# Kernel optimization log

Hardware: AMD Instinct MI355X
Metric: run time of the kernel (lower is better)

The kernel has to match this reference:

```python
import jax, jax.numpy as jnp
import numpy as np

D_MODEL = 512
NUM_HEADS = 8
D_HEAD = 64
BATCH = 2
SEQ = 2048
NEG_BIG = 1.0e10


def setup_inputs() -> dict:
    key = jax.random.key(0)
    k1, k2, k3, k4, k5 = jax.random.split(key, 5)
    scale = D_MODEL ** -0.5
    return {
        "x": jax.random.normal(k1, (BATCH, SEQ, D_MODEL), dtype=jnp.float32),
        "W_Q": jax.random.normal(k2, (NUM_HEADS, D_HEAD, D_MODEL), dtype=jnp.float32) * scale,
        "W_K": jax.random.normal(k3, (NUM_HEADS, D_HEAD, D_MODEL), dtype=jnp.float32) * scale,
        "W_V": jax.random.normal(k4, (NUM_HEADS, D_HEAD, D_MODEL), dtype=jnp.float32) * scale,
        "W_O": jax.random.normal(k5, (D_MODEL, D_HEAD * NUM_HEADS), dtype=jnp.float32) * scale,
    }


def reference(x, W_Q, W_K, W_V, W_O):
    b, n, d = x.shape
    # q,k,v: [b, heads, pos, d_head]
    q = jnp.einsum('ihd,bpd->biph', W_Q, x)
    k = jnp.einsum('ihd,bpd->biph', W_K, x)
    v = jnp.einsum('ihd,bpd->biph', W_V, x)
    # scores: [b, heads, q_pos, k_pos]
    scores = jnp.einsum('biph,biqh->biqp', k, q)
    tril = jnp.tril(jnp.ones((n, n), dtype=scores.dtype))   # keep p <= q
    triu = jnp.triu(jnp.ones((n, n), dtype=scores.dtype))   # buffer 'mask'
    # Faithful to source: tril(scores) - 1e10 * (1 - triu)
    masked = scores * tril - NEG_BIG * (1.0 - triu)
    attn = jax.nn.softmax(masked / (D_HEAD ** 0.5), axis=-1)
    z = jnp.einsum('biph,biqp->biqh', v, attn)               # [b, i, q, h]
    z_flat = jnp.transpose(z, (0, 2, 1, 3)).reshape(b, n, -1)  # [b, q, i*h]
    out = jnp.einsum('df,bqf->bqd', W_O, z_flat)
    return out
```

## Files before the change

### kernel.cpp

```cpp
#include <hip/hip_runtime.h>
#include <stdint.h>

#define BATCH 2
#define SEQ 2048
#define DM 512
#define NH 8
#define DH 64
#define MROWS (BATCH * SEQ)
#define NCHUNK 64
#define CHUNK (SEQ / NCHUNK)

typedef __attribute__((ext_vector_type(8))) short bf16x8;
typedef __attribute__((ext_vector_type(4))) float f32x4;

__device__ __forceinline__ unsigned short f2bf(float f) {
    union { float f; uint32_t u; } x; x.f = f;
    uint32_t r = x.u + 0x7fffu + ((x.u >> 16) & 1u);
    return (unsigned short)(r >> 16);
}
__device__ __forceinline__ float bf2f(unsigned short s) {
    union { uint32_t u; float f; } x; x.u = ((uint32_t)s) << 16;
    return x.f;
}

__device__ __forceinline__ void gl_lds16(const void* g, void* l) {
    __builtin_amdgcn_global_load_lds(
        (const __attribute__((address_space(1))) void*)(uintptr_t)g,
        (__attribute__((address_space(3))) void*)(uint32_t)(uintptr_t)l,
        16, 0, 0);
}

__global__ void cvt_all(const float4* __restrict__ x,
                        const float4* __restrict__ Wq, const float4* __restrict__ Wk,
                        const float4* __restrict__ Wv, const float4* __restrict__ Wo,
                        ushort4* __restrict__ xb, ushort4* __restrict__ wb) {
    int i = blockIdx.x * blockDim.x + threadIdx.x;
    float4 v; ushort4* dst; int off;
    if (i < 524288) {
        v = x[i]; dst = xb; off = i;
    } else {
        int j = i - 524288;
        if (j < 131072) {
            int head = j >> 14, rp = (j >> 7) & 127, colq = j & 127;
            v = (rp < 64) ? Wq[head * 8192 + rp * 128 + colq]
                          : Wk[head * 8192 + (rp - 64) * 128 + colq];
        } else if (j < 196608) {
            v = Wv[j - 131072];
        } else {
            v = Wo[j - 196608];
        }
        dst = wb; off = j;
    }
    ushort4 o; o.x = f2bf(v.x); o.y = f2bf(v.y); o.z = f2bf(v.z); o.w = f2bf(v.w);
    dst[off] = o;
}

__global__ __launch_bounds__(256) void proj(
    const unsigned short* __restrict__ xb, const unsigned short* __restrict__ wb,
    float* __restrict__ cA, float* __restrict__ cW,
    unsigned short* __restrict__ V, float* __restrict__ csum)
{
    __shared__ __align__(16) unsigned short S[4 * 256 * 32];
    const int t = threadIdx.x, lane = t & 63, wave = t >> 6;
    const int lr2 = lane >> 2;
    const int csrc = ((lane & 3) ^ ((lane >> 3) & 3)) * 8;
    const int l15 = lane & 15, q = lane >> 4;
    const int bid = blockIdx.x;
    const int wm = wave * 32;

    if (bid < 256) {
        constexpr int TE = 256 * 32;
        const int head = bid & 7, m0 = (bid >> 3) * 128;
        const unsigned short* Bw = wb + head * 65536;
        const unsigned short* gb[4];
#pragma unroll
        for (int r = 0; r < 4; r++) {
            int g = (r * 4 + wave) * 16 + lr2;
            gb[r] = (g < 128) ? xb + (size_t)(m0 + g) * 512 + csrc
                              : Bw + (size_t)(g - 128) * 512 + csrc;
        }
        int aoff[2], boff[8];
#pragma unroll
        for (int i = 0; i < 2; i++) {
            int R = wm + i * 16 + l15;
            aoff[i] = R * 32 + ((q ^ ((R >> 1) & 3)) * 8);
        }
#pragma unroll
        for (int j = 0; j < 8; j++) {
            int R = 128 + j * 16 + l15;
            boff[j] = R * 32 + ((q ^ ((R >> 1) & 3)) * 8);
        }
        f32x4 acc[2][8];
#pragma unroll
        for (int i = 0; i < 2; i++)
#pragma unroll
            for (int j = 0; j < 8; j++) { f32x4 z = {0.f,0.f,0.f,0.f}; acc[i][j] = z; }

        auto stage = [&](int buf, int tt) {
            const int k0 = tt * 32;
#pragma unroll
            for (int r = 0; r < 4; r++)
                gl_lds16(gb[r] + k0, S + buf * TE + (r * 4 + wave) * 512);
        };
        auto compute = [&](int buf) {
            const unsigned short* Sb = S + buf * TE;
            bf16x8 af[2], bfr[8];
#pragma unroll
            for (int i = 0; i < 2; i++) af[i] = *(const bf16x8*)(Sb + aoff[i]);
#pragma unroll
            for (int j = 0; j < 8; j++) bfr[j] = *(const bf16x8*)(Sb + boff[j]);
            __builtin_amdgcn_s_setprio(1);
#pragma unroll
            for (int i = 0; i < 2; i++)
#pragma unroll
                for (int j = 0; j < 8; j++)
                    acc[i][j] = __builtin_amdgcn_mfma_f32_16x16x32_bf16(af[i], bfr[j], acc[i][j], 0, 0, 0);
            __builtin_amdgcn_s_setprio(0);
        };

        stage(0, 0); stage(1, 1); stage(2, 2);
        for (int tt = 0; tt < 14; ++tt) {
            asm volatile("s_waitcnt vmcnt(8)" ::: "memory");
            __builtin_amdgcn_s_barrier();
            compute(tt & 3);
            if (tt <= 12) stage((tt + 3) & 3, tt + 3);
        }
        asm volatile("s_waitcnt vmcnt(4)" ::: "memory");
        __builtin_amdgcn_s_barrier();
        compute(2);
        asm volatile("s_waitcnt vmcnt(0)" ::: "memory");
        __builtin_amdgcn_s_barrier();
        compute(3);

#pragma unroll
        for (int i = 0; i < 2; i++)
#pragma unroll
            for (int r = 0; r < 4; r++) {
                float d = 0.f;
#pragma unroll
                for (int j = 0; j < 4; j++) d += acc[i][j][r] * acc[i][j + 4][r];
                d += __shfl_xor(d, 1); d += __shfl_xor(d, 2);
                d += __shfl_xor(d, 4); d += __shfl_xor(d, 8);
                if (l15 == 0) {
                    int row = m0 + wm + i * 16 + (lane >> 4) * 4 + r;
                    int p = row & (SEQ - 1);
                    float dd = d * 0.125f;
                    float M = fmaxf(dd, 0.f);
                    float a = expf(dd - M), e0 = expf(-M);
                    float Z = a + (float)(SEQ - 1 - p) * e0;
                    cA[row * NH + head] = a / Z;
                    cW[row * NH + head] = e0 / Z;
                }
            }
    } else {
        constexpr int TE2 = 192 * 32;
        const int b2 = bid - 256;
        const int head = b2 & 7, m0 = (b2 >> 3) * 128, n0 = head * 64;
        const unsigned short* Bv = wb + 524288 + (size_t)n0 * 512;
        const unsigned short* gb[3];
#pragma unroll
        for (int r = 0; r < 3; r++) {
            int g = (r * 4 + wave) * 16 + lr2;
            gb[r] = (g < 128) ? xb + (size_t)(m0 + g) * 512 + csrc
                              : Bv + (size_t)(g - 128) * 512 + csrc;
        }
        int aoff[2], boff[4];
#pragma unroll
        for (int i = 0; i < 2; i++) {
            int R = wm + i * 16 + l15;
            aoff[i] = R * 32 + ((q ^ ((R >> 1) & 3)) * 8);
        }
#pragma unroll
        for (int j = 0; j < 4; j++) {
            int R = 128 + j * 16 + l15;
            boff[j] = R * 32 + ((q ^ ((R >> 1) & 3)) * 8);
        }
        f32x4 acc[2][4];
#pragma unroll
        for (int i = 0; i < 2; i++)
#pragma unroll
            for (int j = 0; j < 4; j++) { f32x4 z = {0.f,0.f,0.f,0.f}; acc[i][j] = z; }

        auto stage = [&](int buf, int tt) {
            const int k0 = tt * 32;
#pragma unroll
            for (int r = 0; r < 3; r++)
                gl_lds16(gb[r] + k0, S + buf * TE2 + (r * 4 + wave) * 512);
        };
        auto compute = [&](int buf) {
            const unsigned short* Sb = S + buf * TE2;
            bf16x8 af[2], bfr[4];
#pragma unroll
            for (int i = 0; i < 2; i++) af[i] = *(const bf16x8*)(Sb + aoff[i]);
#pragma unroll
            for (int j = 0; j < 4; j++) bfr[j] = *(const bf16x8*)(Sb + boff[j]);
            __builtin_amdgcn_s_setprio(1);
#pragma unroll
            for (int i = 0; i < 2; i++)
#pragma unroll
                for (int j = 0; j < 4; j++)
                    acc[i][j] = __builtin_amdgcn_mfma_f32_16x16x32_bf16(af[i], bfr[j], acc[i][j], 0, 0, 0);
            __builtin_amdgcn_s_setprio(0);
        };

        stage(0, 0); stage(1, 1); stage(2, 2);
        for (int tt = 0; tt < 14; ++tt) {
            asm volatile("s_waitcnt vmcnt(6)" ::: "memory");
            __builtin_amdgcn_s_barrier();
            compute(tt & 3);
            if (tt <= 12) stage((tt + 3) & 3, tt + 3);
        }
        asm volatile("s_waitcnt vmcnt(3)" ::: "memory");
        __builtin_amdgcn_s_barrier();
        compute(2);
        asm volatile("s_waitcnt vmcnt(0)" ::: "memory");
        __builtin_amdgcn_s_barrier();
        compute(3);

        const int crow = m0 + wm + (lane >> 4) * 4;
#pragma unroll
        for (int i = 0; i < 2; i++)
#pragma unroll
            for (int j = 0; j < 4; j++)
#pragma unroll
                for (int r = 0; r < 4; r++)
                    V[(size_t)(crow + i * 16 + r) * DM + n0 + j * 16 + l15] = f2bf(acc[i][j][r]);
        float s[4];
#pragma unroll
        for (int j = 0; j < 4; j++) {
            s[j] = 0.f;
#pragma unroll
            for (int i = 0; i < 2; i++)
#pragma unroll
                for (int r = 0; r < 4; r++) s[j] += acc[i][j][r];
            s[j] += __shfl_xor(s[j], 16);
            s[j] += __shfl_xor(s[j], 32);
        }
        if (lane < 16) {
            int bi = (m0 >> 11) * NH + head;
            int chunk = ((m0 & (SEQ - 1)) >> 5) + wave;
#pragma unroll
            for (int j = 0; j < 4; j++)
                csum[(bi * NCHUNK + chunk) * 64 + j * 16 + lane] = s[j];
        }
    }
}

__global__ __launch_bounds__(256) void zbuild(
    const unsigned short* __restrict__ V, const float* __restrict__ csum,
    const float* __restrict__ cA, const float* __restrict__ cW,
    unsigned short* __restrict__ Zb) {
    int ci = blockIdx.x * 4 + (threadIdx.x >> 6);
    int h = threadIdx.x & 63;
    int c = ci & (NCHUNK - 1), bi = ci >> 6;
    int i = bi & 7, b = bi >> 3;
    float r = 0.f;
#pragma unroll 4
    for (int cc = c + 1; cc < NCHUNK; cc++) r += csum[((bi << 6) + cc) * 64 + h];
#pragma unroll 4
    for (int j = CHUNK - 1; j >= 0; j--) {
        int p = c * CHUNK + j;
        size_t row = (size_t)(b * SEQ + p);
        float v = bf2f(V[row * DM + i * DH + h]);
        float a = cA[row * NH + i], w = cW[row * NH + i];
        Zb[row * DM + i * DH + h] = f2bf(fmaf(a, v, w * r));
        r += v;
    }
}

template<int TM, int TN, int WM, int WN>
__global__ __launch_bounds__(256) void gemm_bt(
    const unsigned short* __restrict__ A, const unsigned short* __restrict__ B,
    float* __restrict__ C, int M, int N, int K)
{
    constexpr int ROWS = TM + TN;
    static_assert(ROWS == 128, "pipeline waits assume 128 staged rows");
    constexpr int MI = WM / 16, NJ = WN / 16;
    constexpr int WAVES_N = TN / WN;
    constexpr int TE = ROWS * 32;
    __shared__ __align__(16) unsigned short S[4 * TE];
    const int t = threadIdx.x, lane = t & 63, wave = t >> 6;
    const int wm = (wave / WAVES_N) * WM, wn = (wave % WAVES_N) * WN;
    const int m0 = blockIdx.x * TM, n0 = blockIdx.y * TN;
    const int lr2 = lane >> 2;
    const int csrc = ((lane & 3) ^ ((lane >> 3) & 3)) * 8;
    const int l15 = lane & 15, q = lane >> 4;

    const unsigned short* gb[2];
#pragma unroll
    for (int r = 0; r < 2; r++) {
        int g = (r * 4 + wave) * 16 + lr2;
        gb[r] = (g < TM) ? A + (size_t)(m0 + g) * K + csrc
                         : B + (size_t)(n0 + g - TM) * K + csrc;
    }
    int aoff[MI], boff[NJ];
#pragma unroll
    for (int i = 0; i < MI; i++) {
        int R = wm + i * 16 + l15;
        aoff[i] = R * 32 + ((q ^ ((R >> 1) & 3)) * 8);
    }
#pragma unroll
    for (int j = 0; j < NJ; j++) {
        int R = TM + wn + j * 16 + l15;
        boff[j] = R * 32 + ((q ^ ((R >> 1) & 3)) * 8);
    }

    f32x4 acc[MI][NJ];
#pragma unroll
    for (int i = 0; i < MI; i++)
#pragma unroll
        for (int j = 0; j < NJ; j++) { f32x4 z = {0.f,0.f,0.f,0.f}; acc[i][j] = z; }

    auto stage = [&](int buf, int tt) {
        const int k0 = tt * 32;
#pragma unroll
        for (int r = 0; r < 2; r++)
            gl_lds16(gb[r] + k0, S + buf * TE + (r * 4 + wave) * 512);
    };
    auto compute = [&](int buf) {
        const unsigned short* Sb = S + buf * TE;
        bf16x8 af[MI], bfr[NJ];
#pragma unroll
        for (int i = 0; i < MI; i++) af[i] = *(const bf16x8*)(Sb + aoff[i]);
#pragma unroll
        for (int j = 0; j < NJ; j++) bfr[j] = *(const bf16x8*)(Sb + boff[j]);
        __builtin_amdgcn_s_setprio(1);
#pragma unroll
        for (int i = 0; i < MI; i++)
#pragma unroll
            for (int j = 0; j < NJ; j++)
                acc[i][j] = __builtin_amdgcn_mfma_f32_16x16x32_bf16(af[i], bfr[j], acc[i][j], 0, 0, 0);
        __builtin_amdgcn_s_setprio(0);
    };

    const int NT = K / 32;
    stage(0, 0); stage(1, 1); stage(2, 2);
    for (int tt = 0; tt < NT - 2; ++tt) {
        asm volatile("s_waitcnt vmcnt(4)" ::: "memory");
        __builtin_amdgcn_s_barrier();
        compute(tt & 3);
        if (tt + 3 < NT) stage((tt + 3) & 3, tt + 3);
    }
    asm volatile("s_waitcnt vmcnt(2)" ::: "memory");
    __builtin_amdgcn_s_barrier();
    compute((NT - 2) & 3);
    asm volatile("s_waitcnt vmcnt(0)" ::: "memory");
    __builtin_amdgcn_s_barrier();
    compute((NT - 1) & 3);

    const int crow = m0 + wm + (lane >> 4) * 4;
    const int ccol = n0 + wn + (lane & 15);
#pragma unroll
    for (int i = 0; i < MI; i++)
#pragma unroll
        for (int j = 0; j < NJ; j++)
#pragma unroll
            for (int r = 0; r < 4; r++)
                C[(size_t)(crow + i * 16 + r) * N + ccol + j * 16] = acc[i][j][r];
}

extern "C" void kernel_launch(void* const* d_in, const int* in_sizes, int n_in,
                              void* d_out, int out_size, void* d_ws, size_t ws_size,
                              hipStream_t stream) {
    const float* x  = (const float*)d_in[0];
    const float* Wq = (const float*)d_in[1];
    const float* Wk = (const float*)d_in[2];
    const float* Wv = (const float*)d_in[3];
    const float* Wo = (const float*)d_in[4];
    float* out = (float*)d_out;
    char* ws = (char*)d_ws;

    unsigned short* xb = (unsigned short*)(ws);
    unsigned short* wb = (unsigned short*)(ws + 4194304);
    unsigned short* V  = (unsigned short*)(ws + 6291456);
    float* cA = (float*)(ws + 10485760);
    float* cW = (float*)(ws + 10616832);
    float* cs = (float*)(ws + 10747904);
    unsigned short* Zb = (unsigned short*)(ws + 11010048);

    cvt_all<<<3072, 256, 0, stream>>>((const float4*)x, (const float4*)Wq,
                                      (const float4*)Wk, (const float4*)Wv,
                                      (const float4*)Wo, (ushort4*)xb, (ushort4*)wb);
    proj<<<512, 256, 0, stream>>>(xb, wb, cA, cW, V, cs);
    zbuild<<<256, 256, 0, stream>>>(V, cs, cA, cW, Zb);
    gemm_bt<64, 64, 32, 32><<<dim3(64, 8, 1), 256, 0, stream>>>(
        Zb, wb + 786432, out, MROWS, DM, DM);
}
```

Before: 101.2 us.

## Fuse four kernel launches into one cooperative persistent kernel with grid syncs

Replaces the separate convert, projection, Z-build and output GEMM launches with a single cooperative kernel of 256 blocks of 512 threads, separated by grid.sync barriers. Inside it, the projection phase splits waves into two groups: one computes the QK score coefficients and the other computes V and its chunk sums. The aim is to remove launch gaps and inter-kernel idle time. In exchange it costs grid-wide barriers, only 256 blocks of parallelism per phase, and relies on cooperative launch support, falling back to the old four-kernel path if the launch fails.

```diff
diff --git a/kernel.cpp b/kernel.cpp
--- a/kernel.cpp
+++ b/kernel.cpp
@@ -1,5 +1,8 @@
 #include <hip/hip_runtime.h>
+#include <hip/hip_cooperative_groups.h>
 #include <stdint.h>
+
+namespace cg = cooperative_groups;
 
 #define BATCH 2
 #define SEQ 2048
@@ -28,6 +31,334 @@
         (const __attribute__((address_space(1))) void*)(uintptr_t)g,
         (__attribute__((address_space(3))) void*)(uint32_t)(uintptr_t)l,
         16, 0, 0);
+}
+
+__global__ __launch_bounds__(512, 2) void fused(
+    const float4* __restrict__ x, const float4* __restrict__ Wq,
+    const float4* __restrict__ Wk, const float4* __restrict__ Wv,
+    const float4* __restrict__ Wo,
+    unsigned short* __restrict__ xb, unsigned short* __restrict__ wb,
+    float* __restrict__ cA, float* __restrict__ cW,
+    unsigned short* __restrict__ V, float* __restrict__ csum,
+    unsigned short* __restrict__ Zb, float* __restrict__ out)
+{
+    __shared__ __align__(16) unsigned short S[43008];
+    cg::grid_group grid = cg::this_grid();
+
+    const int t = threadIdx.x, lane = t & 63, wave = t >> 6;
+    const int grp = wave >> 2, w4 = wave & 3;
+    const int bid = blockIdx.x;
+    const int lr2 = lane >> 2;
+    const int csrc = ((lane & 3) ^ ((lane >> 3) & 3)) * 8;
+    const int l15 = lane & 15, q = lane >> 4;
+
+    {
+        ushort4* xbq = (ushort4*)xb;
+        ushort4* wbq = (ushort4*)wb;
+        int tid0 = bid * 512 + t;
+#pragma unroll
+        for (int it = 0; it < 6; ++it) {
+            int i = tid0 + it * 131072;
+            float4 v; ushort4* dst; int off;
+            if (i < 524288) {
+                v = x[i]; dst = xbq; off = i;
+            } else {
+                int j = i - 524288;
+                if (j < 131072) {
+                    int head = j >> 14, rp = (j >> 7) & 127, colq = j & 127;
+                    v = (rp < 64) ? Wq[head * 8192 + rp * 128 + colq]
+                                  : Wk[head * 8192 + (rp - 64) * 128 + colq];
+                } else if (j < 196608) {
+                    v = Wv[j - 131072];
+                } else {
+                    v = Wo[j - 196608];
+                }
+                dst = wbq; off = j;
+            }
+            ushort4 o; o.x = f2bf(v.x); o.y = f2bf(v.y); o.z = f2bf(v.z); o.w = f2bf(v.w);
+            dst[off] = o;
+        }
+    }
+    grid.sync();
+
+    if (grp == 0) {
+        constexpr int TEQ = 256 * 32;
+        const int head = bid & 7, m0 = (bid >> 3) * 128;
+        const unsigned short* Bw = wb + head * 65536;
+        const unsigned short* gb[4];
+#pragma unroll
+        for (int r = 0; r < 4; r++) {
+            int g = (r * 4 + w4) * 16 + lr2;
+            gb[r] = (g < 128) ? xb + (size_t)(m0 + g) * 512 + csrc
+                              : Bw + (size_t)(g - 128) * 512 + csrc;
+        }
+        int aoff[2], boff[8];
+#pragma unroll
+        for (int i = 0; i < 2; i++) {
+            int R = w4 * 32 + i * 16 + l15;
+            aoff[i] = R * 32 + ((q ^ ((R >> 1) & 3)) * 8);
+        }
+#pragma unroll
+        for (int j = 0; j < 8; j++) {
+            int R = 128 + j * 16 + l15;
+            boff[j] = R * 32 + ((q ^ ((R >> 1) & 3)) * 8);
+        }
+        f32x4 acc[2][8];
+#pragma unroll
+        for (int i = 0; i < 2; i++)
+#pragma unroll
+            for (int j = 0; j < 8; j++) { f32x4 z = {0.f,0.f,0.f,0.f}; acc[i][j] = z; }
+
+        auto stage = [&](int buf, int tt) {
+            const int k0 = tt * 32;
+#pragma unroll
+            for (int r = 0; r < 4; r++)
+                gl_lds16(gb[r] + k0, S + buf * TEQ + (r * 4 + w4) * 512);
+        };
+        auto compute = [&](int buf) {
+            const unsigned short* Sb = S + buf * TEQ;
+            bf16x8 af[2], bfr[8];
+#pragma unroll
+            for (int i = 0; i < 2; i++) af[i] = *(const bf16x8*)(Sb + aoff[i]);
+#pragma unroll
+            for (int j = 0; j < 8; j++) bfr[j] = *(const bf16x8*)(Sb + boff[j]);
+            __builtin_amdgcn_s_setprio(1);
+#pragma unroll
+            for (int i = 0; i < 2; i++)
+#pragma unroll
+                for (int j = 0; j < 8; j++)
+                    acc[i][j] = __builtin_amdgcn_mfma_f32_16x16x32_bf16(af[i], bfr[j], acc[i][j], 0, 0, 0);
+            __builtin_amdgcn_s_setprio(0);
+        };
+
+        stage(0, 0); stage(1, 1);
+        for (int tt = 0; tt < 14; ++tt) {
+            asm volatile("s_waitcnt vmcnt(4)" ::: "memory");
+            __builtin_amdgcn_s_barrier();
+            compute(tt % 3);
+            stage((tt + 2) % 3, tt + 2);
+        }
+        asm volatile("s_waitcnt vmcnt(4)" ::: "memory");
+        __builtin_amdgcn_s_barrier();
+        compute(2);
+        asm volatile("s_waitcnt vmcnt(0)" ::: "memory");
+        __builtin_amdgcn_s_barrier();
+        compute(0);
+
+#pragma unroll
+        for (int i = 0; i < 2; i++)
+#pragma unroll
+            for (int r = 0; r < 4; r++) {
+                float d = 0.f;
+#pragma unroll
+                for (int j = 0; j < 4; j++) d += acc[i][j][r] * acc[i][j + 4][r];
+                d += __shfl_xor(d, 1); d += __shfl_xor(d, 2);
+                d += __shfl_xor(d, 4); d += __shfl_xor(d, 8);
+                if (l15 == 0) {
+                    int row = m0 + w4 * 32 + i * 16 + (lane >> 4) * 4 + r;
+                    int p = row & (SEQ - 1);
+                    float dd = d * 0.125f;
+                    float M = fmaxf(dd, 0.f);
+                    float a = expf(dd - M), e0 = expf(-M);
+                    float Z = a + (float)(SEQ - 1 - p) * e0;
+                    cA[row * NH + head] = a / Z;
+                    cW[row * NH + head] = e0 / Z;
+                }
+            }
+    } else {
+        constexpr int TEV = 192 * 32;
+        unsigned short* SV = S + 24576;
+        const int head = bid & 7, m0 = (bid >> 3) * 128, n0 = head * 64;
+        const unsigned short* Bv = wb + 524288 + (size_t)n0 * 512;
+        const unsigned short* gb[3];
+#pragma unroll
+        for (int r = 0; r < 3; r++) {
+            int g = (r * 4 + w4) * 16 + lr2;
+            gb[r] = (g < 128) ? xb + (size_t)(m0 + g) * 512 + csrc
+                              : Bv + (size_t)(g - 128) * 512 + csrc;
+        }
+        int aoff[2], boff[4];
+#pragma unroll
+        for (int i = 0; i < 2; i++) {
+            int R = w4 * 32 + i * 16 + l15;
+            aoff[i] = R * 32 + ((q ^ ((R >> 1) & 3)) * 8);
+        }
+#pragma unroll
+        for (int j = 0; j < 4; j++) {
+            int R = 128 + j * 16 + l15;
+            boff[j] = R * 32 + ((q ^ ((R >> 1) & 3)) * 8);
+        }
+        f32x4 acc[2][4];
+#pragma unroll
+        for (int i = 0; i < 2; i++)
+#pragma unroll
+            for (int j = 0; j < 4; j++) { f32x4 z = {0.f,0.f,0.f,0.f}; acc[i][j] = z; }
+
+        auto stage = [&](int buf, int tt) {
+            const int k0 = tt * 32;
+#pragma unroll
+            for (int r = 0; r < 3; r++)
+                gl_lds16(gb[r] + k0, SV + buf * TEV + (r * 4 + w4) * 512);
+        };
+        auto compute = [&](int buf) {
+            const unsigned short* Sb = SV + buf * TEV;
+            bf16x8 af[2], bfr[4];
+#pragma unroll
+            for (int i = 0; i < 2; i++) af[i] = *(const bf16x8*)(Sb + aoff[i]);
+#pragma unroll
+            for (int j = 0; j < 4; j++) bfr[j] = *(const bf16x8*)(Sb + boff[j]);
+            __builtin_amdgcn_s_setprio(1);
+#pragma unroll
+            for (int i = 0; i < 2; i++)
+#pragma unroll
+                for (int j = 0; j < 4; j++)
+                    acc[i][j] = __builtin_amdgcn_mfma_f32_16x16x32_bf16(af[i], bfr[j], acc[i][j], 0, 0, 0);
+            __builtin_amdgcn_s_setprio(0);
+        };
+
+        stage(0, 0); stage(1, 1);
+        for (int tt = 0; tt < 14; ++tt) {
+            asm volatile("s_waitcnt vmcnt(3)" ::: "memory");
+            __builtin_amdgcn_s_barrier();
+            compute(tt % 3);
+            stage((tt + 2) % 3, tt + 2);
+        }
+        asm volatile("s_waitcnt vmcnt(3)" ::: "memory");
+        __builtin_amdgcn_s_barrier();
+        compute(2);
+        asm volatile("s_waitcnt vmcnt(0)" ::: "memory");
+        __builtin_amdgcn_s_barrier();
+        compute(0);
+
+        const int crow = m0 + w4 * 32 + (lane >> 4) * 4;
+#pragma unroll
+        for (int i = 0; i < 2; i++)
+#pragma unroll
+            for (int j = 0; j < 4; j++)
+#pragma unroll
+                for (int r = 0; r < 4; r++)
+                    V[(size_t)(crow + i * 16 + r) * DM + n0 + j * 16 + l15] = f2bf(acc[i][j][r]);
+        float s[4];
+#pragma unroll
+        for (int j = 0; j < 4; j++) {
+            s[j] = 0.f;
+#pragma unroll
+            for (int i = 0; i < 2; i++)
+#pragma unroll
+                for (int r = 0; r < 4; r++) s[j] += acc[i][j][r];
+            s[j] += __shfl_xor(s[j], 16);
+            s[j] += __shfl_xor(s[j], 32);
+        }
+        if (lane < 16) {
+            int bi = (m0 >> 11) * NH + head;
+            int chunk = ((m0 & (SEQ - 1)) >> 5) + w4;
+#pragma unroll
+            for (int j = 0; j < 4; j++)
+                csum[(bi * NCHUNK + chunk) * 64 + j * 16 + lane] = s[j];
+        }
+    }
+    grid.sync();
+
+    if (wave < 4) {
+        int ci = bid * 4 + wave;
+        int h = lane;
+        int c = ci & (NCHUNK - 1), bi = ci >> 6;
+        int i = bi & 7, b = bi >> 3;
+        float r = 0.f;
+#pragma unroll 4
+        for (int cc = c + 1; cc < NCHUNK; cc++) r += csum[((bi << 6) + cc) * 64 + h];
+#pragma unroll 4
+        for (int j = CHUNK - 1; j >= 0; j--) {
+            int p = c * CHUNK + j;
+            size_t row = (size_t)(b * SEQ + p);
+            float v = bf2f(V[row * DM + i * DH + h]);
+            float a = cA[row * NH + i], w = cW[row * NH + i];
+            Zb[row * DM + i * DH + h] = f2bf(fmaf(a, v, w * r));
+            r += v;
+        }
+    }
+    grid.sync();
+
+    {
+        constexpr int TEG = 128 * 32;
+        unsigned short* SG = S + grp * (3 * TEG);
+        const unsigned short* A = Zb;
+        const unsigned short* B = wb + 786432;
+        const int T = grp * 256 + bid;
+        const int m0 = (T >> 3) * 64, n0 = (T & 7) * 64;
+        const int wm2 = (w4 >> 1) * 32, wn2 = (w4 & 1) * 32;
+
+        const unsigned short* gb[2];
+#pragma unroll
+        for (int r = 0; r < 2; r++) {
+            int g = (r * 4 + w4) * 16 + lr2;
+            gb[r] = (g < 64) ? A + (size_t)(m0 + g) * 512 + csrc
+                             : B + (size_t)(n0 + g - 64) * 512 + csrc;
+        }
+        int aoff[2], boff[2];
+#pragma unroll
+        for (int i = 0; i < 2; i++) {
+            int R = wm2 + i * 16 + l15;
+            aoff[i] = R * 32 + ((q ^ ((R >> 1) & 3)) * 8);
+        }
+#pragma unroll
+        for (int j = 0; j < 2; j++) {
+            int R = 64 + wn2 + j * 16 + l15;
+            boff[j] = R * 32 + ((q ^ ((R >> 1) & 3)) * 8);
+        }
+
+        f32x4 acc[2][2];
+#pragma unroll
+        for (int i = 0; i < 2; i++)
+#pragma unroll
+            for (int j = 0; j < 2; j++) { f32x4 z = {0.f,0.f,0.f,0.f}; acc[i][j] = z; }
+
+        auto stage = [&](int buf, int tt) {
+            const int k0 = tt * 32;
+#pragma unroll
+            for (int r = 0; r < 2; r++)
+                gl_lds16(gb[r] + k0, SG + buf * TEG + (r * 4 + w4) * 512);
+        };
+        auto compute = [&](int buf) {
+            const unsigned short* Sb = SG + buf * TEG;
+            bf16x8 af[2], bfr[2];
+#pragma unroll
+            for (int i = 0; i < 2; i++) af[i] = *(const bf16x8*)(Sb + aoff[i]);
+#pragma unroll
+            for (int j = 0; j < 2; j++) bfr[j] = *(const bf16x8*)(Sb + boff[j]);
+            __builtin_amdgcn_s_setprio(1);
+#pragma unroll
+            for (int i = 0; i < 2; i++)
+#pragma unroll
+                for (int j = 0; j < 2; j++)
+                    acc[i][j] = __builtin_amdgcn_mfma_f32_16x16x32_bf16(af[i], bfr[j], acc[i][j], 0, 0, 0);
+            __builtin_amdgcn_s_setprio(0);
+        };
+
+        stage(0, 0); stage(1, 1);
+        for (int tt = 0; tt < 14; ++tt) {
+            asm volatile("s_waitcnt vmcnt(2)" ::: "memory");
+            __builtin_amdgcn_s_barrier();
+            compute(tt % 3);
+            stage((tt + 2) % 3, tt + 2);
+        }
+        asm volatile("s_waitcnt vmcnt(2)" ::: "memory");
+        __builtin_amdgcn_s_barrier();
+        compute(2);
+        asm volatile("s_waitcnt vmcnt(0)" ::: "memory");
+        __builtin_amdgcn_s_barrier();
+        compute(0);
+
+        const int crow = m0 + wm2 + (lane >> 4) * 4;
+        const int ccol = n0 + wn2 + l15;
+#pragma unroll
+        for (int i = 0; i < 2; i++)
+#pragma unroll
+            for (int j = 0; j < 2; j++)
+#pragma unroll
+                for (int r = 0; r < 4; r++)
+                    out[(size_t)(crow + i * 16 + r) * DM + ccol + j * 16] = acc[i][j][r];
+    }
 }
 
 __global__ void cvt_all(const float4* __restrict__ x,
@@ -362,27 +693,34 @@
 extern "C" void kernel_launch(void* const* d_in, const int* in_sizes, int n_in,
                               void* d_out, int out_size, void* d_ws, size_t ws_size,
                               hipStream_t stream) {
-    const float* x  = (const float*)d_in[0];
-    const float* Wq = (const float*)d_in[1];
-    const float* Wk = (const float*)d_in[2];
-    const float* Wv = (const float*)d_in[3];
-    const float* Wo = (const float*)d_in[4];
-    float* out = (float*)d_out;
+    const float4* x4  = (const float4*)d_in[0];
+    const float4* Wq4 = (const float4*)d_in[1];
+    const float4* Wk4 = (const float4*)d_in[2];
+    const float4* Wv4 = (const float4*)d_in[3];
+    const float4* Wo4 = (const float4*)d_in[4];
+    float* outp = (float*)d_out;
     char* ws = (char*)d_ws;
 
-    unsigned short* xb = (unsigned short*)(ws);
-    unsigned short* wb = (unsigned short*)(ws + 4194304);
-    unsigned short* V  = (unsigned short*)(ws + 6291456);
-    float* cA = (float*)(ws + 10485760);
-    float* cW = (float*)(ws + 10616832);
-    float* cs = (float*)(ws + 10747904);
-    unsigned short* Zb = (unsigned short*)(ws + 11010048);
-
-    cvt_all<<<3072, 256, 0, stream>>>((const float4*)x, (const float4*)Wq,
-                                      (const float4*)Wk, (const float4*)Wv,
-                                      (const float4*)Wo, (ushort4*)xb, (ushort4*)wb);
-    proj<<<512, 256, 0, stream>>>(xb, wb, cA, cW, V, cs);
-    zbuild<<<256, 256, 0, stream>>>(V, cs, cA, cW, Zb);
-    gemm_bt<64, 64, 32, 32><<<dim3(64, 8, 1), 256, 0, stream>>>(
-        Zb, wb + 786432, out, MROWS, DM, DM);
-}
+    unsigned short* xbp = (unsigned short*)(ws);
+    unsigned short* wbp = (unsigned short*)(ws + 4194304);
+    unsigned short* Vp  = (unsigned short*)(ws + 6291456);
+    float* cAp = (float*)(ws + 10485760);
+    float* cWp = (float*)(ws + 10616832);
+    float* csp = (float*)(ws + 10747904);
+    unsigned short* Zbp = (unsigned short*)(ws + 11010048);
+
+    void* args[13] = { &x4, &Wq4, &Wk4, &Wv4, &Wo4,
+                       &xbp, &wbp, &cAp, &cWp, &Vp, &csp, &Zbp, &outp };
+    hipError_t e = hipLaunchCooperativeKernel((const void*)fused,
+                                              dim3(256, 1, 1), dim3(512, 1, 1),
+                                              args, 0, stream);
+    if (e != hipSuccess) {
+        (void)hipGetLastError();
+        cvt_all<<<3072, 256, 0, stream>>>(x4, Wq4, Wk4, Wv4, Wo4,
+                                          (ushort4*)xbp, (ushort4*)wbp);
+        proj<<<512, 256, 0, stream>>>(xbp, wbp, cAp, cWp, Vp, csp);
+        zbuild<<<256, 256, 0, stream>>>(Vp, csp, cAp, cWp, Zbp);
+        gemm_bt<64, 64, 32, 32><<<dim3(64, 8, 1), 256, 0, stream>>>(
+            Zbp, wbp + 786432, outp, MROWS, DM, DM);
+    }
+}
```

Measured after the change: 192.0 us. 1.9x slower.
